# Optimization experiments

Hardware: AMD Instinct MI355X
Metric: run time of the kernel (lower is better)

## Reference

```python
import jax, jax.numpy as jnp
import numpy as np

B, T, I, H, O = 4096, 512, 1, 64, 3

def setup_inputs() -> dict:
    key = jax.random.key(0)
    ks = jax.random.split(key, 7)
    s = 1.0 / np.sqrt(H)  # torch default LSTM init scale
    return {
        "x": jax.random.normal(ks[0], (B, T, I), dtype=jnp.float32),
        "W_ih": jax.random.uniform(ks[1], (4 * H, I), jnp.float32, -s, s),
        "W_hh": jax.random.uniform(ks[2], (4 * H, H), jnp.float32, -s, s),
        "b_ih": jax.random.uniform(ks[3], (4 * H,), jnp.float32, -s, s),
        "b_hh": jax.random.uniform(ks[4], (4 * H,), jnp.float32, -s, s),
        "W_out": jax.random.uniform(ks[5], (O, H), jnp.float32, -s, s),
        "b_out": jax.random.uniform(ks[6], (O,), jnp.float32, -s, s),
    }

def reference(x, W_ih, W_hh, b_ih, b_hh, W_out, b_out):
    # Single-layer LSTM (PyTorch gate order i,f,g,o), zero initial state,
    # then linear head applied to the last hidden state (== r_out[:, -1, :]).
    b = b_ih + b_hh
    Bsz, Hh = x.shape[0], W_hh.shape[1]
    # Precompute input projections for all timesteps: [T, B, 4H]
    x_proj = jnp.einsum('bti,gi->tbg', x, W_ih) + b

    def step(carry, xp_t):
        h, c = carry
        gates = xp_t + h @ W_hh.T  # [B, 4H]
        i, f, g, o = jnp.split(gates, 4, axis=-1)
        c_new = jax.nn.sigmoid(f) * c + jax.nn.sigmoid(i) * jnp.tanh(g)
        h_new = jax.nn.sigmoid(o) * jnp.tanh(c_new)
        return (h_new, c_new), None

    h0 = jnp.zeros((Bsz, Hh), x.dtype)
    (h_last, _), _ = jax.lax.scan(step, (h0, h0), x_proj)
    return h_last @ W_out.T + b_out  # [B, 3]
```

## Files before the change

kernel.cpp:

```cpp
#include <hip/hip_runtime.h>

#define BATCH 4096
#define TT 512
#define HH 64
#define BT 8
#define XS 516
#define HS 72

typedef __attribute__((ext_vector_type(8))) short short8;
typedef __attribute__((ext_vector_type(4))) float floatx4;

__device__ __forceinline__ float sigf(float x) {
    return __builtin_amdgcn_rcpf(1.f + __builtin_amdgcn_exp2f(-1.44269504089f * x));
}
__device__ __forceinline__ float tanhf_(float x) {
    float e = __builtin_amdgcn_exp2f(2.88539008178f * x);
    return 1.f - 2.f * __builtin_amdgcn_rcpf(e + 1.f);
}
__device__ __forceinline__ unsigned short f2bf(float f) {
    unsigned u = __float_as_uint(f);
    u = u + 0x7FFFu + ((u >> 16) & 1u);
    return (unsigned short)(u >> 16);
}

__global__ __launch_bounds__(256, 2) void lstm_kernel(
    const float* __restrict__ x, const float* __restrict__ W_ih,
    const float* __restrict__ W_hh, const float* __restrict__ b_ih,
    const float* __restrict__ b_hh, const float* __restrict__ W_out,
    const float* __restrict__ b_out, float* __restrict__ out)
{
    __shared__ __align__(16) float x_s[BT * XS];
    __shared__ __align__(16) unsigned short hb[2][16 * HS];
    __shared__ __align__(16) float hf[BT * 65];

    const int tid = threadIdx.x;
    const int w = tid >> 6;
    const int l = tid & 63;
    const int q = l >> 4;
    const int c = l & 15;
    const int n = 16 * w + c;
    const int bbase = blockIdx.x * BT;

    for (int i = 0; i < 4; ++i) {
        int flat = i * 256 + tid;
        int row = flat >> 7, c4 = flat & 127;
        const float4* xg = reinterpret_cast<const float4*>(x + (size_t)(bbase + row) * TT);
        float4 v = xg[c4];
        *reinterpret_cast<float4*>(&x_s[row * XS + c4 * 4]) = v;
    }
    for (int i = tid; i < 2 * 16 * HS; i += 256) hb[0][i] = 0;

    short8 bfr[4][2];
    float wih[4], bb[4];
    for (int t = 0; t < 4; ++t) {
        int g = 64 * t + n;
        wih[t] = W_ih[g];
        bb[t] = b_ih[g] + b_hh[g];
        for (int ks = 0; ks < 2; ++ks) {
            const float* wp = W_hh + g * 64 + ks * 32 + q * 8;
            short8 v;
            #pragma unroll
            for (int j = 0; j < 8; ++j) v[j] = (short)f2bf(wp[j]);
            bfr[t][ks] = v;
        }
    }
    float cst[2] = {0.f, 0.f};

    __syncthreads();

    int cur = 0;
    for (int ts = 0; ts < TT; ++ts) {
        const unsigned short* hc = hb[cur];
        short8 a0 = *reinterpret_cast<const short8*>(hc + c * HS + q * 8);
        short8 a1 = *reinterpret_cast<const short8*>(hc + c * HS + q * 8 + 32);

        float x0 = x_s[(2 * q) * XS + ts];
        float x1 = x_s[(2 * q + 1) * XS + ts];

        floatx4 acc[4];
        #pragma unroll
        for (int t = 0; t < 4; ++t) {
            acc[t][0] = fmaf(x0, wih[t], bb[t]);
            acc[t][1] = fmaf(x1, wih[t], bb[t]);
            acc[t][2] = 0.f;
            acc[t][3] = 0.f;
        }

        #pragma unroll
        for (int t = 0; t < 4; ++t) {
            acc[t] = __builtin_amdgcn_mfma_f32_16x16x32_bf16(a0, bfr[t][0], acc[t], 0, 0, 0);
            acc[t] = __builtin_amdgcn_mfma_f32_16x16x32_bf16(a1, bfr[t][1], acc[t], 0, 0, 0);
        }

        unsigned short* hnx = hb[cur ^ 1];
        #pragma unroll
        for (int rr = 0; rr < 2; ++rr) {
            float ig = sigf(acc[0][rr]);
            float fg = sigf(acc[1][rr]);
            float gv = tanhf_(acc[2][rr]);
            float og = sigf(acc[3][rr]);
            float cv = fmaf(fg, cst[rr], ig * gv);
            cst[rr] = cv;
            float hv = og * tanhf_(cv);
            hnx[(4 * q + rr) * HS + n] = f2bf(hv);
            if (ts == TT - 1) hf[(2 * q + rr) * 65 + n] = hv;
        }
        cur ^= 1;
        __syncthreads();
    }

    if (tid < BT * 3) {
        int row = tid / 3, o = tid % 3;
        float s = b_out[o];
        #pragma unroll 8
        for (int k = 0; k < HH; ++k) s = fmaf(hf[row * 65 + k], W_out[o * 64 + k], s);
        out[(size_t)(bbase + row) * 3 + o] = s;
    }
}

extern "C" void kernel_launch(void* const* d_in, const int* in_sizes, int n_in,
                              void* d_out, int out_size, void* d_ws, size_t ws_size,
                              hipStream_t stream) {
    const float* x     = (const float*)d_in[0];
    const float* W_ih  = (const float*)d_in[1];
    const float* W_hh  = (const float*)d_in[2];
    const float* b_ih  = (const float*)d_in[3];
    const float* b_hh  = (const float*)d_in[4];
    const float* W_out = (const float*)d_in[5];
    const float* b_out = (const float*)d_in[6];
    float* out = (float*)d_out;
    hipLaunchKernelGGL(lstm_kernel, dim3(BATCH / BT), dim3(256), 0, stream,
                       x, W_ih, W_hh, b_ih, b_hh, W_out, b_out, out);
}
```

Baseline: 303.8 us.

## Halve batch rows per block to four and double occupancy

Each block now handles 4 batch rows instead of 8, giving twice as many blocks, with launch bounds raised to allow 4 blocks per CU. Each lane computes one row's gate activations per step instead of two, and the x values are loaded as a float4 every four timesteps in an unrolled inner loop. The intent is to spread the latency-bound sequential recurrence over more concurrent blocks so that waves hide each other's MFMA and barrier latency. The cost is that MFMA rows stay mostly unused and more total MFMA work is issued per batch element.

```diff
diff --git a/kernel.cpp b/kernel.cpp
--- a/kernel.cpp
+++ b/kernel.cpp
@@ -3,7 +3,7 @@
 #define BATCH 4096
 #define TT 512
 #define HH 64
-#define BT 8
+#define BT 4
 #define XS 516
 #define HS 72
 
@@ -23,7 +23,7 @@
     return (unsigned short)(u >> 16);
 }
 
-__global__ __launch_bounds__(256, 2) void lstm_kernel(
+__global__ __launch_bounds__(256, 4) void lstm_kernel(
     const float* __restrict__ x, const float* __restrict__ W_ih,
     const float* __restrict__ W_hh, const float* __restrict__ b_ih,
     const float* __restrict__ b_hh, const float* __restrict__ W_out,
@@ -41,7 +41,7 @@
     const int n = 16 * w + c;
     const int bbase = blockIdx.x * BT;
 
-    for (int i = 0; i < 4; ++i) {
+    for (int i = 0; i < 2; ++i) {
         int flat = i * 256 + tid;
         int row = flat >> 7, c4 = flat & 127;
         const float4* xg = reinterpret_cast<const float4*>(x + (size_t)(bbase + row) * TT);
@@ -64,49 +64,45 @@
             bfr[t][ks] = v;
         }
     }
-    float cst[2] = {0.f, 0.f};
+    float cst = 0.f;
+
+    floatx4 acc[4];
+    #pragma unroll
+    for (int t = 0; t < 4; ++t) acc[t] = floatx4{0.f, 0.f, 0.f, 0.f};
 
     __syncthreads();
 
     int cur = 0;
-    for (int ts = 0; ts < TT; ++ts) {
-        const unsigned short* hc = hb[cur];
-        short8 a0 = *reinterpret_cast<const short8*>(hc + c * HS + q * 8);
-        short8 a1 = *reinterpret_cast<const short8*>(hc + c * HS + q * 8 + 32);
+    for (int ts4 = 0; ts4 < TT; ts4 += 4) {
+        float4 xq = *reinterpret_cast<const float4*>(&x_s[q * XS + ts4]);
+        #pragma unroll
+        for (int u = 0; u < 4; ++u) {
+            const unsigned short* hc = hb[cur];
+            short8 a0 = *reinterpret_cast<const short8*>(hc + c * HS + q * 8);
+            short8 a1 = *reinterpret_cast<const short8*>(hc + c * HS + q * 8 + 32);
 
-        float x0 = x_s[(2 * q) * XS + ts];
-        float x1 = x_s[(2 * q + 1) * XS + ts];
+            float xv = (&xq.x)[u];
+            #pragma unroll
+            for (int t = 0; t < 4; ++t) acc[t][0] = fmaf(xv, wih[t], bb[t]);
 
-        floatx4 acc[4];
-        #pragma unroll
-        for (int t = 0; t < 4; ++t) {
-            acc[t][0] = fmaf(x0, wih[t], bb[t]);
-            acc[t][1] = fmaf(x1, wih[t], bb[t]);
-            acc[t][2] = 0.f;
-            acc[t][3] = 0.f;
+            #pragma unroll
+            for (int t = 0; t < 4; ++t) {
+                acc[t] = __builtin_amdgcn_mfma_f32_16x16x32_bf16(a0, bfr[t][0], acc[t], 0, 0, 0);
+                acc[t] = __builtin_amdgcn_mfma_f32_16x16x32_bf16(a1, bfr[t][1], acc[t], 0, 0, 0);
+            }
+
+            float ig = sigf(acc[0][0]);
+            float fg = sigf(acc[1][0]);
+            float gv = tanhf_(acc[2][0]);
+            float og = sigf(acc[3][0]);
+            float cv = fmaf(fg, cst, ig * gv);
+            cst = cv;
+            float hv = og * tanhf_(cv);
+            hb[cur ^ 1][(4 * q) * HS + n] = f2bf(hv);
+            if (ts4 + u == TT - 1) hf[q * 65 + n] = hv;
+            cur ^= 1;
+            __syncthreads();
         }
-
-        #pragma unroll
-        for (int t = 0; t < 4; ++t) {
-            acc[t] = __builtin_amdgcn_mfma_f32_16x16x32_bf16(a0, bfr[t][0], acc[t], 0, 0, 0);
-            acc[t] = __builtin_amdgcn_mfma_f32_16x16x32_bf16(a1, bfr[t][1], acc[t], 0, 0, 0);
-        }
-
-        unsigned short* hnx = hb[cur ^ 1];
-        #pragma unroll
-        for (int rr = 0; rr < 2; ++rr) {
-            float ig = sigf(acc[0][rr]);
-            float fg = sigf(acc[1][rr]);
-            float gv = tanhf_(acc[2][rr]);
-            float og = sigf(acc[3][rr]);
-            float cv = fmaf(fg, cst[rr], ig * gv);
-            cst[rr] = cv;
-            float hv = og * tanhf_(cv);
-            hnx[(4 * q + rr) * HS + n] = f2bf(hv);
-            if (ts == TT - 1) hf[(2 * q + rr) * 65 + n] = hv;
-        }
-        cur ^= 1;
-        __syncthreads();
     }
 
     if (tid < BT * 3) {
```

Result: no change. 302.2 us (-0.5%).
